# Optimization experiments

Hardware: AMD Instinct MI355X
Metric: run time of the kernel (lower is better)

The kernel has to match this reference:

```python
import jax, jax.numpy as jnp
import numpy as np

B, D, H, O, RH, P = 8192, 784, 2048, 1024, 128, 64
NI = NJ = NK = 4  # input regions / hidden groups / output groups


def _make_groups():
    idx = np.arange(28 * 28).reshape(28, 28)
    input_groups = np.stack([
        idx[:14, :14].ravel(), idx[:14, 14:].ravel(),
        idx[14:, :14].ravel(), idx[14:, 14:].ravel(),
    ]).astype(np.int32)                                   # [4, 196]
    hidden_groups = np.arange(H, dtype=np.int32).reshape(NJ, H // NJ)   # [4, 512]
    output_groups = np.arange(O, dtype=np.int32).reshape(NK, O // NK)   # [4, 256]
    return input_groups, hidden_groups, output_groups


def setup_inputs() -> dict:
    key = jax.random.key(0)
    ks = jax.random.split(key, 9)
    ig, hg, og = _make_groups()
    inp = {
        "x":   jax.random.normal(ks[0], (B, D), jnp.float32),
        "W1":  jax.random.normal(ks[1], (H, D), jnp.float32) / np.sqrt(D),
        "b1":  jax.random.normal(ks[2], (H,), jnp.float32) * 0.01,
        "W2":  jax.random.normal(ks[3], (O, H), jnp.float32) / np.sqrt(H),
        "b2":  jax.random.normal(ks[4], (O,), jnp.float32) * 0.01,
        "Wr1": jax.random.normal(ks[5], (RH, D), jnp.float32) / np.sqrt(D),
        "br1": jax.random.normal(ks[6], (RH,), jnp.float32) * 0.01,
        "Wr2": jax.random.normal(ks[7], (P, RH), jnp.float32) / np.sqrt(RH),
        "br2": jax.random.normal(ks[8], (P,), jnp.float32) * 0.01,
        "input_groups": jnp.asarray(ig),
        "hidden_groups": jnp.asarray(hg),
        "output_groups": jnp.asarray(og),
        "top_k": 8,
    }
    return inp


def reference(x, W1, b1, W2, b2, Wr1, br1, Wr2, br2,
              input_groups, hidden_groups, output_groups, top_k):
    # --- router MLP (eval mode: dropout = identity, no routing noise) ---
    h_r = jax.nn.relu(x @ Wr1.T + br1)
    scores = h_r @ Wr2.T + br2                      # [B, P]
    probs = jax.nn.softmax(scores, axis=-1)         # temperature = 1.0

    # --- top-k pathway selection + renormalization ---
    top_vals, top_idx = jax.lax.top_k(probs, top_k)
    bsz = x.shape[0]
    mask = jnp.zeros_like(probs).at[jnp.arange(bsz)[:, None], top_idx].set(top_vals)
    wts = mask / (mask.sum(axis=-1, keepdims=True) + 1e-8)
    wts4 = wts.reshape(bsz, NI, NJ, NK)             # pathway_idx = i*16 + j*4 + k

    # --- gather pathway sub-blocks ---
    x_reg = x[:, input_groups]                      # [B, I, 196]
    # W1g[i, j] = W1[hidden_groups[j]][:, input_groups[i]] -> [I, J, 512, 196]
    W1g = W1[hidden_groups[None, :, :, None], input_groups[:, None, None, :]]
    b1g = b1[hidden_groups]                         # [J, 512]
    # W2g[j, k] = W2[output_groups[k]][:, hidden_groups[j]] -> [J, K, 256, 512]
    W2g = W2[output_groups[None, :, :, None], hidden_groups[:, None, None, :]]
    b2g = b2[output_groups]                         # [K, 256]

    # --- pathway computation (exact erf GELU, as torch F.gelu default) ---
    hidden = jax.nn.gelu(
        jnp.einsum('bin,ijhn->ijbh', x_reg, W1g) + b1g[None, :, None, :],
        approximate=False)                          # [I, J, B, 512]
    # weighted pathway outputs, contracted over i, j, h without materializing
    # the full [I, J, K, B, 256] tensor
    out_main = jnp.einsum('ijbh,jkoh,bijk->bko', hidden, W2g, wts4)  # [B, K, 256]
    wsum = wts4.sum(axis=(1, 2))                    # [B, K] (bias weighted per pathway)
    out_blocks = out_main + wsum[:, :, None] * b2g[None]

    out = jnp.zeros((bsz, O), x.dtype).at[:, output_groups].add(out_blocks)
    return out
```

## Files before the change

### kernel.cpp

```cpp
#include <hip/hip_runtime.h>
#include <hip/hip_bf16.h>
#include <hip/hip_fp16.h>

#define B_  8192
#define D_  784
#define H_  2048
#define O_  1024
#define RH_ 128
#define P_  64
#define KP  224
#define KR  800

typedef __attribute__((ext_vector_type(8))) short short8;
typedef __attribute__((ext_vector_type(8))) _Float16 h16x8;
typedef __attribute__((ext_vector_type(4))) float f32x4;

__device__ inline float bf2f(unsigned short u) {
  union { unsigned int i; float f; } v; v.i = ((unsigned int)u) << 16; return v.f;
}
__device__ inline unsigned short f2bf(float f) {
  __hip_bfloat16 h = __float2bfloat16(f);
  return *reinterpret_cast<unsigned short*>(&h);
}
__device__ inline unsigned short f2h(float f) {
  __half h = __float2half(f);
  return *reinterpret_cast<unsigned short*>(&h);
}
__device__ inline float h2f(unsigned short u) {
  __half h = *reinterpret_cast<__half*>(&u);
  return __half2float(h);
}
__device__ inline float erf_fast(float x) {
  float ax = fabsf(x);
  float t = 1.0f / (1.0f + 0.3275911f * ax);
  float p = ((((1.061405429f * t - 1.453152027f) * t + 1.421413741f) * t
              - 0.284496736f) * t + 0.254829592f) * t;
  float y = 1.0f - p * __expf(-ax * ax);
  return x < 0.f ? -y : y;
}
__device__ inline float gelu_exact(float v) {
  return 0.5f * v * (1.0f + erf_fast(v * 0.70710678118654752f));
}

__device__ inline void gload_lds16(const void* g, void* l) {
  __builtin_amdgcn_global_load_lds((const __attribute__((address_space(1))) void*)g,
                                   (__attribute__((address_space(3))) void*)l, 16, 0, 0);
}

template <bool F16>
__device__ inline void gemm128_db(const unsigned short* gA0, const unsigned short* gA1,
                                  const unsigned short* gB0, const unsigned short* gB1,
                                  int K, char* lds, f32x4 acc[4][4]) {
  const int t = threadIdx.x;
  const int w = t >> 6, l = t & 63;
  const int wr = (w >> 1) * 64, wc = (w & 1) * 64;
  const int lr = l & 15;
  const int swr = (lr >> 1) & 3;
  const int arow = (wr + lr) * 64 + (((l >> 4) ^ swr) * 16);
  const int brow = 8192 + (wc + lr) * 64 + (((l >> 4) ^ swr) * 16);
  const int tOff = t * 16;
  {
    char* d = lds + tOff;
    gload_lds16(gA0, d);
    gload_lds16(gA1, d + 4096);
    gload_lds16(gB0, d + 8192);
    gload_lds16(gB1, d + 12288);
  }
  int cur = 0;
  for (int kt = 0; kt < K; kt += 32) {
    const int nxt = kt + 32;
    if (nxt < K) {
      char* d = lds + ((cur ^ 1) << 14) + tOff;
      gload_lds16(gA0 + nxt, d);
      gload_lds16(gA1 + nxt, d + 4096);
      gload_lds16(gB0 + nxt, d + 8192);
      gload_lds16(gB1 + nxt, d + 12288);
      __builtin_amdgcn_sched_barrier(0);
      asm volatile("s_waitcnt vmcnt(4)" ::: "memory");
    } else {
      __builtin_amdgcn_sched_barrier(0);
      asm volatile("s_waitcnt vmcnt(0)" ::: "memory");
    }
    __builtin_amdgcn_sched_barrier(0);
    __builtin_amdgcn_s_barrier();
    __builtin_amdgcn_sched_barrier(0);
    const char* buf = lds + (cur << 14);
    short8 af[4], bfr[4];
#pragma unroll
    for (int f = 0; f < 4; ++f) {
      af[f]  = *(const short8*)(buf + arow + f * 1024);
      bfr[f] = *(const short8*)(buf + brow + f * 1024);
    }
#pragma unroll
    for (int fm = 0; fm < 4; ++fm)
#pragma unroll
      for (int fn = 0; fn < 4; ++fn) {
        if constexpr (F16)
          acc[fm][fn] = __builtin_amdgcn_mfma_f32_16x16x32_f16(
              (h16x8)af[fm], (h16x8)bfr[fn], acc[fm][fn], 0, 0, 0);
        else
          acc[fm][fn] = __builtin_amdgcn_mfma_f32_16x16x32_bf16(af[fm], bfr[fn], acc[fm][fn], 0, 0, 0);
      }
    __builtin_amdgcn_sched_barrier(0);
    __builtin_amdgcn_s_barrier();
    __builtin_amdgcn_sched_barrier(0);
    cur ^= 1;
  }
}

__device__ inline void gemm128_db64(const unsigned short* gA0, const unsigned short* gA1,
                                    const unsigned short* gB0, const unsigned short* gB1,
                                    int K, char* lds, f32x4 acc[4][4]) {
  const int t = threadIdx.x;
  const int w = t >> 6, l = t & 63;
  const int wr = (w >> 1) * 64, wc = (w & 1) * 64;
  const int lr = l & 15;
  const int swr = (lr >> 1) & 3;
  const int arow = (wr + lr) * 64 + (((l >> 4) ^ swr) * 16);
  const int brow = 8192 + (wc + lr) * 64 + (((l >> 4) ^ swr) * 16);
  const int tOff = t * 16;
#define STAGE64(bufbase, ksrc) { \
    char* d = lds + (bufbase) + tOff; \
    gload_lds16(gA0 + (ksrc), d); \
    gload_lds16(gA1 + (ksrc), d + 4096); \
    gload_lds16(gB0 + (ksrc), d + 8192); \
    gload_lds16(gB1 + (ksrc), d + 12288); \
    gload_lds16(gA0 + (ksrc) + 32, d + 16384); \
    gload_lds16(gA1 + (ksrc) + 32, d + 16384 + 4096); \
    gload_lds16(gB0 + (ksrc) + 32, d + 16384 + 8192); \
    gload_lds16(gB1 + (ksrc) + 32, d + 16384 + 12288); \
  }
  STAGE64(0, 0);
  int cur = 0;
  for (int kt = 0; kt < K; kt += 64) {
    if (kt + 64 < K) {
      STAGE64((cur ^ 1) << 15, kt + 64);
      __builtin_amdgcn_sched_barrier(0);
      asm volatile("s_waitcnt vmcnt(8)" ::: "memory");
    } else {
      __builtin_amdgcn_sched_barrier(0);
      asm volatile("s_waitcnt vmcnt(0)" ::: "memory");
    }
    __builtin_amdgcn_sched_barrier(0);
    __builtin_amdgcn_s_barrier();
    __builtin_amdgcn_sched_barrier(0);
    const char* buf = lds + (cur << 15);
#pragma unroll
    for (int c = 0; c < 2; ++c) {
      const char* ch = buf + c * 16384;
      short8 af[4], bfr[4];
#pragma unroll
      for (int f = 0; f < 4; ++f) {
        af[f]  = *(const short8*)(ch + arow + f * 1024);
        bfr[f] = *(const short8*)(ch + brow + f * 1024);
      }
#pragma unroll
      for (int fm = 0; fm < 4; ++fm)
#pragma unroll
        for (int fn = 0; fn < 4; ++fn)
          acc[fm][fn] = __builtin_amdgcn_mfma_f32_16x16x32_bf16(af[fm], bfr[fn], acc[fm][fn], 0, 0, 0);
    }
    __builtin_amdgcn_sched_barrier(0);
    __builtin_amdgcn_s_barrier();
    __builtin_amdgcn_sched_barrier(0);
    cur ^= 1;
  }
#undef STAGE64
}

__device__ inline void gemm128_bt64(const unsigned short* __restrict__ A,
                                    const unsigned short* __restrict__ Bm,
                                    int K, char* lds, f32x4 acc[4][4]) {
  const int t = threadIdx.x;
  const int s_orig = (t & 3) ^ ((t >> 3) & 3);
  const size_t srcOff = (size_t)(t >> 2) * K + s_orig * 8;
  gemm128_db64(A + srcOff, A + srcOff + (size_t)64 * K,
               Bm + srcOff, Bm + srcOff + (size_t)64 * K, K, lds, acc);
}

__global__ void k_prep(const float* __restrict__ x, const float* __restrict__ W1,
                       const float* __restrict__ W2, const int* __restrict__ ig,
                       const float* __restrict__ Wr1,
                       unsigned short* __restrict__ xreg, unsigned short* __restrict__ w1g,
                       unsigned short* __restrict__ w2b,
                       unsigned short* __restrict__ xsp, unsigned short* __restrict__ wr1sp) {
  const size_t N1 = (size_t)4 * B_ * KP;
  const size_t N2 = (size_t)4 * H_ * KP;
  const size_t N3 = (size_t)O_ * H_;
  const size_t N4 = (size_t)B_ * KR;
  const size_t N5 = (size_t)RH_ * KR;
  const size_t TOT = N1 + N2 + N3 + N4 + N5;
  for (size_t idx = (size_t)blockIdx.x * blockDim.x + threadIdx.x; idx < TOT;
       idx += (size_t)gridDim.x * blockDim.x) {
    if (idx < N1) {
      int n = (int)(idx % KP); size_t r = idx / KP;
      int b = (int)(r % B_); int i = (int)(r / B_);
      float v = (n < 196) ? x[(size_t)b * D_ + ig[i * 196 + n]] : 0.f;
      xreg[idx] = f2bf(v);
    } else if (idx < N1 + N2) {
      size_t q = idx - N1;
      int n = (int)(q % KP); size_t r = q / KP;
      int h = (int)(r % H_); int i = (int)(r / H_);
      float v = (n < 196) ? W1[(size_t)h * D_ + ig[i * 196 + n]] : 0.f;
      w1g[q] = f2bf(v);
    } else if (idx < N1 + N2 + N3) {
      size_t q = idx - N1 - N2;
      w2b[q] = f2bf(W2[q]);
    } else if (idx < N1 + N2 + N3 + N4) {
      size_t q = idx - N1 - N2 - N3;
      int c = (int)(q % KR); int b = (int)(q / KR);
      float v = (c < D_) ? x[(size_t)b * D_ + c] : 0.f;
      unsigned short hi = f2h(v);
      unsigned short lo = f2h(v - h2f(hi));
      xsp[(size_t)b * (2 * KR) + c]      = hi;
      xsp[(size_t)b * (2 * KR) + KR + c] = lo;
    } else {
      size_t q = idx - N1 - N2 - N3 - N4;
      int c = (int)(q % KR); int h = (int)(q / KR);
      float v = (c < D_) ? Wr1[(size_t)h * D_ + c] : 0.f;
      unsigned short hi = f2h(v);
      unsigned short lo = f2h(v - h2f(hi));
      wr1sp[(size_t)h * KR + c]                    = hi;
      wr1sp[(size_t)RH_ * KR + h * KR + c]         = hi;
      wr1sp[(size_t)2 * RH_ * KR + h * KR + c]     = lo;
    }
  }
}

__global__ __launch_bounds__(256) void k_r1m(const unsigned short* __restrict__ xsp,
    const unsigned short* __restrict__ wr1sp, float* __restrict__ hrp) {
  __shared__ __align__(128) char lds[32768];
  const int mt = blockIdx.x, z = blockIdx.y;
  const int t = threadIdx.x;
  const int aoff = (z == 1) ? KR : 0;
  const int s_orig = (t & 3) ^ ((t >> 3) & 3);
  const int scol = s_orig * 8;
  const unsigned short* gA0 = xsp + ((size_t)(mt * 128) + (t >> 2)) * (2 * KR) + aoff + scol;
  const unsigned short* gA1 = gA0 + (size_t)64 * (2 * KR);
  const unsigned short* gB0 = wr1sp + (size_t)z * RH_ * KR + (size_t)(t >> 2) * KR + scol;
  const unsigned short* gB1 = gB0 + (size_t)64 * KR;
  f32x4 acc[4][4];
#pragma unroll
  for (int a = 0; a < 4; ++a)
#pragma unroll
    for (int b = 0; b < 4; ++b) acc[a][b] = (f32x4){0.f, 0.f, 0.f, 0.f};
  gemm128_db<true>(gA0, gA1, gB0, gB1, KR, lds, acc);
  float* hz = hrp + (size_t)z * B_ * RH_;
  const int w = t >> 6, l = t & 63;
  const int rbase = mt * 128 + (w >> 1) * 64 + (l >> 4) * 4;
  const int cb = (w & 1) * 64 + (l & 15);
#pragma unroll
  for (int fn = 0; fn < 4; ++fn) {
    const int h = cb + fn * 16;
#pragma unroll
    for (int fm = 0; fm < 4; ++fm)
#pragma unroll
      for (int r = 0; r < 4; ++r)
        hz[(size_t)(rbase + fm * 16 + r) * RH_ + h] = acc[fm][fn][r];
  }
}

#define R2S 32
__global__ __launch_bounds__(256) void k_r2(const float* __restrict__ hrp,
    const float* __restrict__ br1,
    const float* __restrict__ Wr2, const float* __restrict__ br2,
    float* __restrict__ wts, float* __restrict__ wsum,
    unsigned long long* __restrict__ actmask) {
  __shared__ float Ws[64][130];
  __shared__ float hs[R2S][128];
  const int s0 = blockIdx.x * R2S;
  const int t = threadIdx.x;
  for (int idx = t; idx < 2048; idx += 256) {
    int r = idx >> 5, c = (idx & 31) * 4;
    *(float4*)&Ws[r][c] = *(const float4*)(Wr2 + (size_t)r * RH_ + c);
  }
  for (int idx = t; idx < R2S * 32; idx += 256) {
    int r = idx >> 5, c = (idx & 31) * 4;
    const size_t off = (size_t)(s0 + r) * RH_ + c;
    float4 p0 = *(const float4*)(hrp + off);
    float4 p1 = *(const float4*)(hrp + (size_t)1 * B_ * RH_ + off);
    float4 p2 = *(const float4*)(hrp + (size_t)2 * B_ * RH_ + off);
    float4 bb = *(const float4*)(br1 + c);
    float4 s;
    s.x = fmaxf(p0.x + p1.x + p2.x + bb.x, 0.f);
    s.y = fmaxf(p0.y + p1.y + p2.y + bb.y, 0.f);
    s.z = fmaxf(p0.z + p1.z + p2.z + bb.z, 0.f);
    s.w = fmaxf(p0.w + p1.w + p2.w + bb.w, 0.f);
    *(float4*)&hs[r][c] = s;
  }
  __syncthreads();
  const int w = t >> 6, p = t & 63;
  const float wb2 = br2[p];
  for (int si = 0; si < R2S / 4; ++si) {
    const int sl = w * (R2S / 4) + si;
    float sc = wb2;
#pragma unroll
    for (int kk = 0; kk < 32; ++kk) {
      float4 h4 = *(const float4*)&hs[sl][kk * 4];
      float4 w4 = *(const float4*)&Ws[p][kk * 4];
      sc += h4.x * w4.x + h4.y * w4.y + h4.z * w4.z + h4.w * w4.w;
    }
    float m = sc;
#pragma unroll
    for (int o = 32; o; o >>= 1) m = fmaxf(m, __shfl_xor(m, o));
    float e = __expf(sc - m);
    float Z = e;
#pragma unroll
    for (int o = 32; o; o >>= 1) Z += __shfl_xor(Z, o);
    bool sel = false;
    float ssum = 0.f;
    for (int it = 0; it < 8; ++it) {
      float v = sel ? -1.f : e;
      float vm = v;
#pragma unroll
      for (int o = 32; o; o >>= 1) vm = fmaxf(vm, __shfl_xor(vm, o));
      unsigned long long mask = __ballot(!sel && v == vm);
      int first = __ffsll((long long)mask) - 1;
      if (p == first) sel = true;
      ssum += vm;
    }
    const float dn = 1.0f / (ssum + 1e-8f * Z);
    const float wv = sel ? e * dn : 0.f;
    wts[(size_t)(s0 + sl) * 64 + p] = wv;
    const unsigned long long am = __ballot(sel);
    if (p == 0) actmask[s0 + sl] = am;
    float part = wv;
#pragma unroll
    for (int o = 4; o < 64; o <<= 1) part += __shfl_xor(part, o);
    if (p < 4) wsum[(size_t)(s0 + sl) * 4 + p] = part;
  }
}

__global__ __launch_bounds__(256) void k_compact(const unsigned long long* __restrict__ actmask,
                                                 int* __restrict__ lists,
                                                 int* __restrict__ counts) {
  __shared__ int wcnt[4];
  __shared__ int sbase;
  const int ij = blockIdx.x;
  const int shift = (ij >> 2) * 16 + (ij & 3) * 4;
  const int t = threadIdx.x;
  const int wid = t >> 6, lane = t & 63;
  unsigned long long mk[32];
#pragma unroll
  for (int c = 0; c < 32; ++c) mk[c] = actmask[c * 256 + t];
  if (t == 0) sbase = 0;
  __syncthreads();
  for (int c = 0; c < 32; ++c) {
    const int b = c * 256 + t;
    const bool act = ((mk[c] >> shift) & 0xFULL) != 0ULL;
    const unsigned long long m = __ballot(act);
    if (lane == 0) wcnt[wid] = __popcll(m);
    __syncthreads();
    int off = sbase;
    const int tot = wcnt[0] + wcnt[1] + wcnt[2] + wcnt[3];
    for (int q = 0; q < wid; ++q) off += wcnt[q];
    if (act)
      lists[ij * B_ + off + __popcll(m & ((1ULL << lane) - 1ULL))] = b;
    __syncthreads();
    if (t == 0) sbase += tot;
  }
  __syncthreads();
  if (t == 0) counts[ij] = sbase;
}

__global__ __launch_bounds__(256) void k_l1g(const unsigned short* __restrict__ xreg,
    const unsigned short* __restrict__ w1g, const float* __restrict__ b1,
    const int* __restrict__ lists, const int* __restrict__ counts,
    unsigned short* __restrict__ hid16) {
  const int id = blockIdx.x;
  const int xcd = id & 7;
  const int within = id >> 3;
  const int ij = xcd * 2 + (within >> 8);
  const int sub = within & 255;
  const int mt = sub >> 2;
  const int ntl = sub & 3;
  const int iq = ij >> 2;
  const int nt = (ij & 3) * 4 + ntl;
  const int count = counts[ij];
  if (mt * 128 >= count) return;
  __shared__ __align__(128) char lds[32768];
  __shared__ int rows[128];
  const int t = threadIdx.x;
  const int* list = lists + (size_t)ij * B_;
  if (t < 128) {
    int rl = mt * 128 + t;
    rows[t] = list[rl < count ? rl : count - 1];
  }
  __syncthreads();
  const int s_orig = (t & 3) ^ ((t >> 3) & 3);
  const int scol = s_orig * 8;
  const int r0 = rows[t >> 2], r1 = rows[(t >> 2) + 64];
  const unsigned short* gA0 = xreg + ((size_t)iq * B_ + r0) * KP + scol;
  const unsigned short* gA1 = xreg + ((size_t)iq * B_ + r1) * KP + scol;
  const unsigned short* gB0 = w1g + ((size_t)(iq * H_ + nt * 128) + (t >> 2)) * KP + scol;
  const unsigned short* gB1 = gB0 + (size_t)64 * KP;
  f32x4 acc[4][4];
#pragma unroll
  for (int a = 0; a < 4; ++a)
#pragma unroll
    for (int b = 0; b < 4; ++b) acc[a][b] = (f32x4){0.f, 0.f, 0.f, 0.f};
  gemm128_db<false>(gA0, gA1, gB0, gB1, KP, lds, acc);
  const int w = t >> 6, l = t & 63;
  const int rloc0 = (w >> 1) * 64 + (l >> 4) * 4;
  const int cloc = (w & 1) * 64 + (l & 15);
  unsigned short* lt = (unsigned short*)lds;
  __syncthreads();
#pragma unroll
  for (int fn = 0; fn < 4; ++fn) {
    const int col = cloc + fn * 16;
    const float bias = b1[nt * 128 + col];
#pragma unroll
    for (int fm = 0; fm < 4; ++fm)
#pragma unroll
      for (int r = 0; r < 4; ++r) {
        const int row = rloc0 + fm * 16 + r;
        const int gsw = (col >> 3) ^ (row & 7);
        lt[row * 128 + gsw * 8 + (col & 7)] = f2h(acc[fm][fn][r] + bias);
      }
  }
  __syncthreads();
  const int mlim = count - mt * 128;
  const int row = t >> 1, half = t & 1;
  if (row < mlim) {
    unsigned short* dst = hid16 + ((size_t)iq * B_ + rows[row]) * H_ + nt * 128 + half * 64;
#pragma unroll
    for (int q = 0; q < 8; ++q) {
      const int g = (half * 8 + q) ^ (row & 7);
      *(short8*)(dst + q * 8) = *(const short8*)(lt + row * 128 + g * 8);
    }
  }
}

__global__ __launch_bounds__(256) void k_combine(unsigned short* __restrict__ hid,
                                                 const float* __restrict__ wts) {
  const int b = blockIdx.x;
  const int n = threadIdx.x * 8;
  const int j = n >> 9;
  const float* wb = wts + (size_t)b * 64 + j * 4;
  float acc[4][8];
#pragma unroll
  for (int k = 0; k < 4; ++k)
#pragma unroll
    for (int e = 0; e < 8; ++e) acc[k][e] = 0.f;
#pragma unroll
  for (int i = 0; i < 4; ++i) {
    const float4 w4 = *(const float4*)(wb + i * 16);
    if (w4.x != 0.f || w4.y != 0.f || w4.z != 0.f || w4.w != 0.f) {
      short8 raw = *(const short8*)(hid + ((size_t)i * B_ + b) * H_ + n);
#pragma unroll
      for (int e = 0; e < 8; ++e) {
        float g = gelu_exact(h2f((unsigned short)raw[e]));
        acc[0][e] += g * w4.x;
        acc[1][e] += g * w4.y;
        acc[2][e] += g * w4.z;
        acc[3][e] += g * w4.w;
      }
    }
  }
#pragma unroll
  for (int k = 0; k < 4; ++k) {
    short8 outv;
#pragma unroll
    for (int e = 0; e < 8; ++e) outv[e] = (short)f2bf(acc[k][e]);
    *(short8*)(hid + ((size_t)k * B_ + b) * H_ + n) = outv;
  }
}

__global__ __launch_bounds__(256) void k_l2(const unsigned short* __restrict__ G,
    const unsigned short* __restrict__ w2b, const float* __restrict__ b2,
    const float* __restrict__ wsum, float* __restrict__ out) {
  __shared__ __align__(128) char lds[65536];
  const int id = blockIdx.x;
  const int xcd = id & 7, mt = id >> 3;
  const int nt = xcd & 1, k = xcd >> 1;
  const unsigned short* A  = G + ((size_t)k * B_ + mt * 128) * H_;
  const unsigned short* Bm = w2b + ((size_t)(k * 256 + nt * 128)) * H_;
  f32x4 acc[4][4];
#pragma unroll
  for (int a = 0; a < 4; ++a)
#pragma unroll
    for (int b = 0; b < 4; ++b) acc[a][b] = (f32x4){0.f, 0.f, 0.f, 0.f};
  gemm128_bt64(A, Bm, H_, lds, acc);
  const int t = threadIdx.x, w = t >> 6, l = t & 63;
  const int rbase = mt * 128 + (w >> 1) * 64 + (l >> 4) * 4;
  const int cb = nt * 128 + (w & 1) * 64 + (l & 15);
#pragma unroll
  for (int fn = 0; fn < 4; ++fn) {
    const int ncol = k * 256 + cb + fn * 16;
    const float bias = b2[ncol];
#pragma unroll
    for (int fm = 0; fm < 4; ++fm)
#pragma unroll
      for (int r = 0; r < 4; ++r) {
        const int m = rbase + fm * 16 + r;
        out[(size_t)m * O_ + ncol] = acc[fm][fn][r] + wsum[m * 4 + k] * bias;
      }
  }
}

extern "C" void kernel_launch(void* const* d_in, const int* in_sizes, int n_in,
                              void* d_out, int out_size, void* d_ws, size_t ws_size,
                              hipStream_t stream) {
  const float* x   = (const float*)d_in[0];
  const float* W1  = (const float*)d_in[1];
  const float* b1  = (const float*)d_in[2];
  const float* W2  = (const float*)d_in[3];
  const float* b2  = (const float*)d_in[4];
  const float* Wr1 = (const float*)d_in[5];
  const float* br1 = (const float*)d_in[6];
  const float* Wr2 = (const float*)d_in[7];
  const float* br2 = (const float*)d_in[8];
  const int*   ig  = (const int*)d_in[9];
  float* out = (float*)d_out;
  char* ws = (char*)d_ws;
  unsigned short* xreg = (unsigned short*)(ws);
  unsigned short* w1g  = (unsigned short*)(ws + 14680064);
  unsigned short* w2b  = (unsigned short*)(ws + 18350080);
  float*          wts  = (float*)(ws + 22544384);
  float*          wsum = (float*)(ws + 24641536);
  unsigned short* hid  = (unsigned short*)(ws + 24772608);
  float*          hrp   = (float*)(ws + 24772608);
  unsigned short* xsp   = (unsigned short*)(ws + 24772608 + 12582912);
  unsigned short* wr1sp = (unsigned short*)(ws + 24772608 + 38797312);
  int*                lists   = (int*)d_out;
  int*                counts  = lists + 16 * B_;
  unsigned long long* actmask = (unsigned long long*)((char*)d_out + 524352);

  k_prep<<<dim3(2048), dim3(256), 0, stream>>>(x, W1, W2, ig, Wr1, xreg, w1g, w2b, xsp, wr1sp);
  k_r1m<<<dim3(B_ / 128, 3), dim3(256), 0, stream>>>(xsp, wr1sp, hrp);
  k_r2<<<dim3(B_ / R2S), dim3(256), 0, stream>>>(hrp, br1, Wr2, br2, wts, wsum, actmask);
  k_compact<<<dim3(16), dim3(256), 0, stream>>>(actmask, lists, counts);
  k_l1g<<<dim3(4096), dim3(256), 0, stream>>>(xreg, w1g, b1, lists, counts, hid);
  k_combine<<<dim3(B_), dim3(256), 0, stream>>>(hid, wts);
  k_l2<<<dim3(512), dim3(256), 0, stream>>>(hid, w2b, b2, wsum, out);
}
```

Measured before the change: 208.9 us.

## Fuse fp16 hi/lo split of x and Wr1 into router GEMM loads

The router first-layer GEMM now reads fp32 x and Wr1 directly, converts them to fp16 hi or lo parts in registers and writes them to LDS. This replaces the separate prep pass that wrote the split xsp and wr1sp arrays to global memory, so that pass's write and re-read traffic is gone. In exchange, each of the three z blocks redoes the conversion, and the loads are plain register loads with manual double buffering. The layer-2 block-index mapping also changes from XCD-interleaved to grouping consecutive M tiles, which alters L2 locality. An unused gemm128_bt helper is added.

```diff
diff --git a/kernel.cpp b/kernel.cpp
--- a/kernel.cpp
+++ b/kernel.cpp
@@ -178,18 +178,24 @@
                Bm + srcOff, Bm + srcOff + (size_t)64 * K, K, lds, acc);
 }
 
+__device__ inline void gemm128_bt(const unsigned short* __restrict__ A,
+                                  const unsigned short* __restrict__ Bm,
+                                  int K, char* lds, f32x4 acc[4][4]) {
+  const int t = threadIdx.x;
+  const int s_orig = (t & 3) ^ ((t >> 3) & 3);
+  const size_t srcOff = (size_t)(t >> 2) * K + s_orig * 8;
+  gemm128_db<false>(A + srcOff, A + srcOff + (size_t)64 * K,
+                    Bm + srcOff, Bm + srcOff + (size_t)64 * K, K, lds, acc);
+}
+
 __global__ void k_prep(const float* __restrict__ x, const float* __restrict__ W1,
                        const float* __restrict__ W2, const int* __restrict__ ig,
-                       const float* __restrict__ Wr1,
                        unsigned short* __restrict__ xreg, unsigned short* __restrict__ w1g,
-                       unsigned short* __restrict__ w2b,
-                       unsigned short* __restrict__ xsp, unsigned short* __restrict__ wr1sp) {
+                       unsigned short* __restrict__ w2b) {
   const size_t N1 = (size_t)4 * B_ * KP;
   const size_t N2 = (size_t)4 * H_ * KP;
   const size_t N3 = (size_t)O_ * H_;
-  const size_t N4 = (size_t)B_ * KR;
-  const size_t N5 = (size_t)RH_ * KR;
-  const size_t TOT = N1 + N2 + N3 + N4 + N5;
+  const size_t TOT = N1 + N2 + N3;
   for (size_t idx = (size_t)blockIdx.x * blockDim.x + threadIdx.x; idx < TOT;
        idx += (size_t)gridDim.x * blockDim.x) {
     if (idx < N1) {
@@ -203,50 +209,97 @@
       int h = (int)(r % H_); int i = (int)(r / H_);
       float v = (n < 196) ? W1[(size_t)h * D_ + ig[i * 196 + n]] : 0.f;
       w1g[q] = f2bf(v);
-    } else if (idx < N1 + N2 + N3) {
+    } else {
       size_t q = idx - N1 - N2;
       w2b[q] = f2bf(W2[q]);
-    } else if (idx < N1 + N2 + N3 + N4) {
-      size_t q = idx - N1 - N2 - N3;
-      int c = (int)(q % KR); int b = (int)(q / KR);
-      float v = (c < D_) ? x[(size_t)b * D_ + c] : 0.f;
-      unsigned short hi = f2h(v);
-      unsigned short lo = f2h(v - h2f(hi));
-      xsp[(size_t)b * (2 * KR) + c]      = hi;
-      xsp[(size_t)b * (2 * KR) + KR + c] = lo;
-    } else {
-      size_t q = idx - N1 - N2 - N3 - N4;
-      int c = (int)(q % KR); int h = (int)(q / KR);
-      float v = (c < D_) ? Wr1[(size_t)h * D_ + c] : 0.f;
-      unsigned short hi = f2h(v);
-      unsigned short lo = f2h(v - h2f(hi));
-      wr1sp[(size_t)h * KR + c]                    = hi;
-      wr1sp[(size_t)RH_ * KR + h * KR + c]         = hi;
-      wr1sp[(size_t)2 * RH_ * KR + h * KR + c]     = lo;
-    }
-  }
-}
-
-__global__ __launch_bounds__(256) void k_r1m(const unsigned short* __restrict__ xsp,
-    const unsigned short* __restrict__ wr1sp, float* __restrict__ hrp) {
+    }
+  }
+}
+
+__global__ __launch_bounds__(256) void k_r1m(const float* __restrict__ x,
+    const float* __restrict__ Wr1, float* __restrict__ hrp) {
   __shared__ __align__(128) char lds[32768];
   const int mt = blockIdx.x, z = blockIdx.y;
   const int t = threadIdx.x;
-  const int aoff = (z == 1) ? KR : 0;
+  const int row = t >> 2;
   const int s_orig = (t & 3) ^ ((t >> 3) & 3);
-  const int scol = s_orig * 8;
-  const unsigned short* gA0 = xsp + ((size_t)(mt * 128) + (t >> 2)) * (2 * KR) + aoff + scol;
-  const unsigned short* gA1 = gA0 + (size_t)64 * (2 * KR);
-  const unsigned short* gB0 = wr1sp + (size_t)z * RH_ * KR + (size_t)(t >> 2) * KR + scol;
-  const unsigned short* gB1 = gB0 + (size_t)64 * KR;
+  const bool aLo = (z == 1), bLo = (z == 2);
+  const float* xa0 = x + (size_t)(mt * 128 + row) * D_;
+  const float* xa1 = x + (size_t)(mt * 128 + 64 + row) * D_;
+  const float* wb0 = Wr1 + (size_t)row * D_;
+  const float* wb1 = Wr1 + (size_t)(64 + row) * D_;
+  const int w = t >> 6, l = t & 63;
+  const int wr = (w >> 1) * 64, wc = (w & 1) * 64;
+  const int lr = l & 15;
+  const int swr = (lr >> 1) & 3;
+  const int arow = (wr + lr) * 64 + (((l >> 4) ^ swr) * 16);
+  const int brow = 8192 + (wc + lr) * 64 + (((l >> 4) ^ swr) * 16);
   f32x4 acc[4][4];
 #pragma unroll
   for (int a = 0; a < 4; ++a)
 #pragma unroll
     for (int b = 0; b < 4; ++b) acc[a][b] = (f32x4){0.f, 0.f, 0.f, 0.f};
-  gemm128_db<true>(gA0, gA1, gB0, gB1, KR, lds, acc);
+
+  float4 R[8];
+  const float4 Z4 = {0.f, 0.f, 0.f, 0.f};
+#define R1M_LOAD(kt) { \
+    const int c0 = (kt) + s_orig * 8; \
+    const bool v0 = (c0 + 4 <= D_), v1 = (c0 + 8 <= D_); \
+    R[0] = v0 ? *(const float4*)(xa0 + c0) : Z4; \
+    R[1] = v1 ? *(const float4*)(xa0 + c0 + 4) : Z4; \
+    R[2] = v0 ? *(const float4*)(xa1 + c0) : Z4; \
+    R[3] = v1 ? *(const float4*)(xa1 + c0 + 4) : Z4; \
+    R[4] = v0 ? *(const float4*)(wb0 + c0) : Z4; \
+    R[5] = v1 ? *(const float4*)(wb0 + c0 + 4) : Z4; \
+    R[6] = v0 ? *(const float4*)(wb1 + c0) : Z4; \
+    R[7] = v1 ? *(const float4*)(wb1 + c0 + 4) : Z4; \
+  }
+#define R1M_CVTW(bufbase) { \
+    char* d = lds + (bufbase) + t * 16; \
+    short8 s0, s1, s2, s3; \
+    const float* fr = (const float*)R; \
+    for (int e = 0; e < 8; ++e) { \
+      float va = fr[e], vb = fr[8 + e], vc = fr[16 + e], vd = fr[24 + e]; \
+      unsigned short ha = f2h(va), hb = f2h(vb), hc = f2h(vc), hd = f2h(vd); \
+      s0[e] = (short)(aLo ? f2h(va - h2f(ha)) : ha); \
+      s1[e] = (short)(aLo ? f2h(vb - h2f(hb)) : hb); \
+      s2[e] = (short)(bLo ? f2h(vc - h2f(hc)) : hc); \
+      s3[e] = (short)(bLo ? f2h(vd - h2f(hd)) : hd); \
+    } \
+    *(short8*)(d)         = s0; \
+    *(short8*)(d + 4096)  = s1; \
+    *(short8*)(d + 8192)  = s2; \
+    *(short8*)(d + 12288) = s3; \
+  }
+  R1M_LOAD(0);
+  R1M_CVTW(0);
+  R1M_LOAD(32);
+  __syncthreads();
+  int cur = 0;
+  for (int kt = 0; kt < KR; kt += 32) {
+    const char* buf = lds + (cur << 14);
+    short8 af[4], bfr[4];
+#pragma unroll
+    for (int f = 0; f < 4; ++f) {
+      af[f]  = *(const short8*)(buf + arow + f * 1024);
+      bfr[f] = *(const short8*)(buf + brow + f * 1024);
+    }
+#pragma unroll
+    for (int fm = 0; fm < 4; ++fm)
+#pragma unroll
+      for (int fn = 0; fn < 4; ++fn)
+        acc[fm][fn] = __builtin_amdgcn_mfma_f32_16x16x32_f16(
+            (h16x8)af[fm], (h16x8)bfr[fn], acc[fm][fn], 0, 0, 0);
+    if (kt + 32 < KR) {
+      R1M_CVTW((cur ^ 1) << 14);
+      if (kt + 64 < KR) R1M_LOAD(kt + 64);
+    }
+    __syncthreads();
+    cur ^= 1;
+  }
+#undef R1M_LOAD
+#undef R1M_CVTW
   float* hz = hrp + (size_t)z * B_ * RH_;
-  const int w = t >> 6, l = t & 63;
   const int rbase = mt * 128 + (w >> 1) * 64 + (l >> 4) * 4;
   const int cb = (w & 1) * 64 + (l & 15);
 #pragma unroll
@@ -471,8 +524,8 @@
     const float* __restrict__ wsum, float* __restrict__ out) {
   __shared__ __align__(128) char lds[65536];
   const int id = blockIdx.x;
-  const int xcd = id & 7, mt = id >> 3;
-  const int nt = xcd & 1, k = xcd >> 1;
+  const int grp = id >> 6, mt = id & 63;
+  const int nt = grp & 1, k = grp >> 1;
   const unsigned short* A  = G + ((size_t)k * B_ + mt * 128) * H_;
   const unsigned short* Bm = w2b + ((size_t)(k * 256 + nt * 128)) * H_;
   f32x4 acc[4][4];
@@ -519,15 +572,13 @@
   float*          wts  = (float*)(ws + 22544384);
   float*          wsum = (float*)(ws + 24641536);
   unsigned short* hid  = (unsigned short*)(ws + 24772608);
-  float*          hrp   = (float*)(ws + 24772608);
-  unsigned short* xsp   = (unsigned short*)(ws + 24772608 + 12582912);
-  unsigned short* wr1sp = (unsigned short*)(ws + 24772608 + 38797312);
+  float*          hrp  = (float*)(ws + 24772608);
   int*                lists   = (int*)d_out;
   int*                counts  = lists + 16 * B_;
   unsigned long long* actmask = (unsigned long long*)((char*)d_out + 524352);
 
-  k_prep<<<dim3(2048), dim3(256), 0, stream>>>(x, W1, W2, ig, Wr1, xreg, w1g, w2b, xsp, wr1sp);
-  k_r1m<<<dim3(B_ / 128, 3), dim3(256), 0, stream>>>(xsp, wr1sp, hrp);
+  k_prep<<<dim3(2048), dim3(256), 0, stream>>>(x, W1, W2, ig, xreg, w1g, w2b);
+  k_r1m<<<dim3(B_ / 128, 3), dim3(256), 0, stream>>>(x, Wr1, hrp);
   k_r2<<<dim3(B_ / R2S), dim3(256), 0, stream>>>(hrp, br1, Wr2, br2, wts, wsum, actmask);
   k_compact<<<dim3(16), dim3(256), 0, stream>>>(actmask, lists, counts);
   k_l1g<<<dim3(4096), dim3(256), 0, stream>>>(xreg, w1g, b1, lists, counts, hid);
```

Result: slower. 216.2 us (+3.5%).
